# Kernel optimization log

Hardware: AMD Instinct MI355X
Metric: run time of the kernel (lower is better)

The kernel has to match this reference:

```python
import jax, jax.numpy as jnp
import numpy as np

N, E, D = 20000, 320000, 512


def _gat(x, W, a_src, a_dst, bias, src, dst, n, heads, ch):
    # PyG GATConv (eval mode, add_self_loops already applied via src/dst)
    h = (x @ W).reshape(n, heads, ch)              # [n, H, C]
    es = (h * a_src).sum(-1)                       # [n, H]
    ed = (h * a_dst).sum(-1)                       # [n, H]
    e = jax.nn.leaky_relu(es[src] + ed[dst], 0.2)  # [E, H]
    # edge-softmax grouped by destination node
    m = jax.ops.segment_max(e, dst, num_segments=n)
    ex = jnp.exp(e - m[dst])
    z = jax.ops.segment_sum(ex, dst, num_segments=n)
    alpha = ex / (z[dst] + 1e-16)                  # [E, H]
    out = jax.ops.segment_sum(h[src] * alpha[:, :, None], dst, num_segments=n)
    return out.reshape(n, heads * ch) + bias


def _ln(x, g, b):
    mu = x.mean(-1, keepdims=True)
    v = ((x - mu) ** 2).mean(-1, keepdims=True)
    return (x - mu) * jax.lax.rsqrt(v + 1e-5) * g + b


def setup_inputs() -> dict:
    key = jax.random.key(0)
    ks = jax.random.split(key, 24)
    p = lambda k, shape: jax.random.normal(k, shape, dtype=jnp.float32) * 0.05
    inp = {
        'x': jax.random.normal(ks[0], (N, D), dtype=jnp.float32),
        'edge_index': jax.random.randint(ks[1], (2, E), 0, N, dtype=jnp.int32),
        # GAT layer 1: 512 -> 8 heads x 128
        'w1': p(ks[2], (D, 1024)), 'as1': p(ks[3], (8, 128)), 'ad1': p(ks[4], (8, 128)), 'b1': jnp.zeros((1024,), jnp.float32),
        'g1': jnp.ones((1024,), jnp.float32), 'be1': jnp.zeros((1024,), jnp.float32),
        # GAT layer 2: 1024 -> 4 heads x 64
        'w2': p(ks[5], (1024, 256)), 'as2': p(ks[6], (4, 64)), 'ad2': p(ks[7], (4, 64)), 'b2': jnp.zeros((256,), jnp.float32),
        'g2': jnp.ones((256,), jnp.float32), 'be2': jnp.zeros((256,), jnp.float32),
        # GAT layer 3: 256 -> 2 heads x 32
        'w3': p(ks[8], (256, 64)), 'as3': p(ks[9], (2, 32)), 'ad3': p(ks[10], (2, 32)), 'b3': jnp.zeros((64,), jnp.float32),
        'g3': jnp.ones((64,), jnp.float32), 'be3': jnp.zeros((64,), jnp.float32),
        # anomaly scorer MLP
        'sw1': p(ks[11], (64, 64)), 'sb1': jnp.zeros((64,), jnp.float32),
        'sg1': jnp.ones((64,), jnp.float32), 'sbe1': jnp.zeros((64,), jnp.float32),
        'sw2': p(ks[12], (64, 32)), 'sb2': jnp.zeros((32,), jnp.float32),
        'sg2': jnp.ones((32,), jnp.float32), 'sbe2': jnp.zeros((32,), jnp.float32),
        'sw3': p(ks[13], (32, 1)), 'sb3': jnp.zeros((1,), jnp.float32),
    }
    return inp


def reference(x, edge_index, w1, as1, ad1, b1, g1, be1,
              w2, as2, ad2, b2, g2, be2,
              w3, as3, ad3, b3, g3, be3,
              sw1, sb1, sg1, sbe1, sw2, sb2, sg2, sbe2, sw3, sb3):
    loops = jnp.arange(N, dtype=edge_index.dtype)
    src = jnp.concatenate([edge_index[0], loops])  # add self-loops (PyG default)
    dst = jnp.concatenate([edge_index[1], loops])

    h1 = jax.nn.relu(_gat(x, w1, as1, ad1, b1, src, dst, N, 8, 128))
    h1 = _ln(h1, g1, be1)
    h2 = jax.nn.relu(_gat(h1, w2, as2, ad2, b2, src, dst, N, 4, 64))
    h2 = _ln(h2, g2, be2)
    h2 = h2 + h1[:, :256]
    h3 = jax.nn.relu(_gat(h2, w3, as3, ad3, b3, src, dst, N, 2, 32))
    h3 = _ln(h3, g3, be3)
    h3 = h3 + h2[:, :64]

    s = jax.nn.relu(h3 @ sw1 + sb1)
    s = _ln(s, sg1, sbe1)
    s = jax.nn.relu(s @ sw2 + sb2)
    s = _ln(s, sg2, sbe2)
    return jax.nn.sigmoid(s @ sw3 + sb3)  # [N, 1]
```

## Files before the change

kernel.cpp:

```cpp
#include <hip/hip_runtime.h>
#include <hip/hip_bf16.h>
#include <hip/hip_fp16.h>
#include <cstdint>

#define NN 20000
#define EE 320000
#define ETOT (EE + NN)

using f32x4 = __attribute__((ext_vector_type(4))) float;
using f16x8 = __attribute__((ext_vector_type(8))) _Float16;
typedef unsigned short ushortT;

__global__ __launch_bounds__(256) void preproc_kernel(
    const float* __restrict__ x, __half* __restrict__ x16,
    const float* __restrict__ w1, ushortT* __restrict__ w1t,
    const float* __restrict__ w2, ushortT* __restrict__ w2t,
    const float* __restrict__ w3, ushortT* __restrict__ w3t,
    const int* __restrict__ ei, int* __restrict__ deg)
{
  constexpr int N0 = NN * 512;
  constexpr int N1 = 512 * 1024;
  constexpr int N2 = 1024 * 256;
  constexpr int N3 = 256 * 64;
  constexpr int TOT = N0 + N1 + N2 + N3 + ETOT;
  for (int i = blockIdx.x * 256 + threadIdx.x; i < TOT; i += gridDim.x * 256) {
    int j = i;
    if (j < N0) { x16[j] = __float2half(x[j]); continue; }
    j -= N0;
    if (j < N1) {
      int k = j >> 10, c = j & 1023;
      w1t[(size_t)c * 512 + k] = __half_as_ushort(__float2half(w1[j]));
      continue;
    }
    j -= N1;
    if (j < N2) {
      int k = j >> 8, c = j & 255;
      w2t[(size_t)c * 1024 + k] = __half_as_ushort(__float2half(w2[j]));
      continue;
    }
    j -= N2;
    if (j < N3) {
      int k = j >> 6, c = j & 63;
      w3t[(size_t)c * 256 + k] = __half_as_ushort(__float2half(w3[j]));
      continue;
    }
    j -= N3;
    int d = (j < EE) ? ei[EE + j] : (j - EE);
    atomicAdd(&deg[d], 1);
  }
}

__global__ __launch_bounds__(1024) void scan_kernel(const int* __restrict__ deg,
                                                    int* __restrict__ row_ptr,
                                                    int* __restrict__ cursor) {
  __shared__ int partial[1024];
  const int t = threadIdx.x;
  constexpr int PER = (NN + 1023) / 1024;
  const int base = t * PER;
  int vals[PER];
  int local = 0;
  #pragma unroll
  for (int j = 0; j < PER; ++j) {
    int i = base + j;
    int v = (i < NN) ? deg[i] : 0;
    vals[j] = v; local += v;
  }
  partial[t] = local;
  __syncthreads();
  for (int off = 1; off < 1024; off <<= 1) {
    int x = (t >= off) ? partial[t - off] : 0;
    __syncthreads();
    partial[t] += x;
    __syncthreads();
  }
  int prefix = partial[t] - local;
  #pragma unroll
  for (int j = 0; j < PER; ++j) {
    int i = base + j;
    if (i < NN) { row_ptr[i] = prefix; cursor[i] = prefix; }
    prefix += vals[j];
  }
  if (t == 1023) row_ptr[NN] = prefix;
}

__global__ void scatter_kernel(const int* __restrict__ ei, int* __restrict__ cursor,
                               int* __restrict__ csr_src) {
  int i = blockIdx.x * 256 + threadIdx.x;
  if (i >= ETOT) return;
  int s, d;
  if (i < EE) { s = ei[i]; d = ei[EE + i]; } else { s = d = i - EE; }
  int pos = atomicAdd(&cursor[d], 1);
  csr_src[pos] = s;
}

__device__ __forceinline__ void gload16(const void* g, void* l) {
  __builtin_amdgcn_global_load_lds((const __attribute__((address_space(1))) void*)g,
                                   (__attribute__((address_space(3))) void*)l, 16, 0, 0);
}

template<int N> __device__ __forceinline__ void wait_vm() {
  if constexpr (N == 0) asm volatile("s_waitcnt vmcnt(0)" ::: "memory");
  else if constexpr (N == 2) asm volatile("s_waitcnt vmcnt(2)" ::: "memory");
  else if constexpr (N == 3) asm volatile("s_waitcnt vmcnt(3)" ::: "memory");
  else if constexpr (N == 4) asm volatile("s_waitcnt vmcnt(4)" ::: "memory");
  else if constexpr (N == 6) asm volatile("s_waitcnt vmcnt(6)" ::: "memory");
  else if constexpr (N == 8) asm volatile("s_waitcnt vmcnt(8)" ::: "memory");
  else static_assert(N <= 8, "unsupported vmcnt");
}

template<int BM, int BN, int FM, int FN, int CHEAD>
__global__ __launch_bounds__(256) void gemm_f16(
    const __half* __restrict__ A,
    const ushortT* __restrict__ Bt,
    __half* __restrict__ C, int M, int Ncols, int K,
    const float* __restrict__ asrc, const float* __restrict__ adst,
    float* __restrict__ es_g, float* __restrict__ ed_g, int H)
{
  constexpr int BK   = 32;
  constexpr int HALF = (BM + BN) * BK;
  constexpr int NL   = (BM * 4 + BN * 4) / 256;
  __shared__ ushortT lds[2 * HALF];

  const int tid  = threadIdx.x;
  const int lane = tid & 63;
  const int wid  = tid >> 6;
  const int wm   = (wid >> 1) * (FM * 16);
  const int wn   = (wid & 1) * (FN * 16);
  const int row0 = blockIdx.x * BM;
  const int col0 = blockIdx.y * BN;
  const int r    = lane & 15;
  const int kg   = lane >> 4;

  const ushortT* Au = (const ushortT*)A;

  auto STAGE = [&](int buf, int k0) {
    ushortT* sA = lds + buf * HALF;
    ushortT* sB = sA + BM * BK;
    #pragma unroll
    for (int i = tid; i < BM * 4; i += 256) {
      int row = i >> 2, slot = i & 3;
      int gs = slot ^ (row & 3);
      int grow = row0 + row; if (grow > M - 1) grow = M - 1;
      gload16(Au + (size_t)grow * K + k0 + gs * 8, sA + row * BK + slot * 8);
    }
    #pragma unroll
    for (int i = tid; i < BN * 4; i += 256) {
      int row = i >> 2, slot = i & 3;
      int gs = slot ^ (row & 3);
      gload16(Bt + (size_t)(col0 + row) * K + k0 + gs * 8, sB + row * BK + slot * 8);
    }
  };

  f32x4 acc[FM][FN] = {};
  const int nt = K / BK;

  STAGE(0, 0);
  for (int t = 0; t < nt; ++t) {
    if (t + 1 < nt) { STAGE((t + 1) & 1, (t + 1) * BK); wait_vm<NL>(); }
    else            { wait_vm<0>(); }
    __builtin_amdgcn_s_barrier();
    __builtin_amdgcn_sched_barrier(0);

    const ushortT* sA = lds + (t & 1) * HALF;
    const ushortT* sB = sA + BM * BK;
    const int ks = (kg ^ (r & 3)) * 8;
    f16x8 a[FM], b[FN];
    #pragma unroll
    for (int mi = 0; mi < FM; ++mi)
      a[mi] = *(const f16x8*)(sA + (wm + mi * 16 + r) * BK + ks);
    #pragma unroll
    for (int ni = 0; ni < FN; ++ni)
      b[ni] = *(const f16x8*)(sB + (wn + ni * 16 + r) * BK + ks);
    #pragma unroll
    for (int mi = 0; mi < FM; ++mi)
      #pragma unroll
      for (int ni = 0; ni < FN; ++ni)
        acc[mi][ni] = __builtin_amdgcn_mfma_f32_16x16x32_f16(a[mi], b[ni], acc[mi][ni], 0, 0, 0);
    __builtin_amdgcn_sched_barrier(0);
    __builtin_amdgcn_s_barrier();
  }

  #pragma unroll
  for (int mi = 0; mi < FM; ++mi) {
    int rb = row0 + wm + mi * 16 + (lane >> 4) * 4;
    #pragma unroll
    for (int ni = 0; ni < FN; ++ni) {
      int cc = col0 + wn + ni * 16 + (lane & 15);
      #pragma unroll
      for (int j = 0; j < 4; ++j) {
        int rr = rb + j;
        if (rr < M) C[(size_t)rr * Ncols + cc] = __float2half(acc[mi][ni][j]);
      }
    }
  }

  constexpr bool DIRECT = (CHEAD == FN * 16);
  float av[FN], dv[FN];
  #pragma unroll
  for (int ni = 0; ni < FN; ++ni) {
    int cc = col0 + wn + ni * 16 + (lane & 15);
    av[ni] = asrc[cc];
    dv[ni] = adst[cc];
  }
  float ps[FM][4], pd[FM][4];
  #pragma unroll
  for (int mi = 0; mi < FM; ++mi)
    #pragma unroll
    for (int j = 0; j < 4; ++j) {
      float s = 0.f, d = 0.f;
      #pragma unroll
      for (int ni = 0; ni < FN; ++ni) {
        float v = acc[mi][ni][j];
        s += v * av[ni];
        d += v * dv[ni];
      }
      #pragma unroll
      for (int off = 8; off; off >>= 1) {
        s += __shfl_xor(s, off);
        d += __shfl_xor(d, off);
      }
      ps[mi][j] = s; pd[mi][j] = d;
    }
  const int head = (col0 + wn) / CHEAD;
  if constexpr (DIRECT) {
    if ((lane & 15) == 0) {
      #pragma unroll
      for (int mi = 0; mi < FM; ++mi)
        #pragma unroll
        for (int j = 0; j < 4; ++j) {
          int rr = row0 + wm + mi * 16 + (lane >> 4) * 4 + j;
          if (rr < M) { es_g[rr * H + head] = ps[mi][j]; ed_g[rr * H + head] = pd[mi][j]; }
        }
    }
  } else {
    float* l_es = (float*)lds;
    float* l_ed = l_es + BM;
    __syncthreads();
    if ((wid & 1) == 0 && (lane & 15) == 0) {
      #pragma unroll
      for (int mi = 0; mi < FM; ++mi)
        #pragma unroll
        for (int j = 0; j < 4; ++j) {
          int rl = wm + mi * 16 + (lane >> 4) * 4 + j;
          l_es[rl] = ps[mi][j]; l_ed[rl] = pd[mi][j];
        }
    }
    __syncthreads();
    if ((wid & 1) == 1 && (lane & 15) == 0) {
      #pragma unroll
      for (int mi = 0; mi < FM; ++mi)
        #pragma unroll
        for (int j = 0; j < 4; ++j) {
          int rl = wm + mi * 16 + (lane >> 4) * 4 + j;
          int rr = row0 + rl;
          if (rr < M) {
            es_g[rr * H + head] = ps[mi][j] + l_es[rl];
            ed_g[rr * H + head] = pd[mi][j] + l_ed[rl];
          }
        }
    }
  }
}

template<int VPT> struct GVec;
template<> struct GVec<16> { uint4 a, b; };
template<> struct GVec<4>  { uint2 a; };
template<> struct GVec<1>  { ushortT a; };

template<int VPT>
__device__ __forceinline__ GVec<VPT> gload(const __half* p) {
  GVec<VPT> v;
  if constexpr (VPT == 16) { v.a = *(const uint4*)p; v.b = *(const uint4*)(p + 8); }
  else if constexpr (VPT == 4) { v.a = *(const uint2*)p; }
  else { v.a = *(const ushortT*)p; }
  return v;
}

template<int VPT>
__device__ __forceinline__ void gfma(const GVec<VPT>& u, float w, float* acc) {
  if constexpr (VPT == 1) {
    __half hv;
    *(ushortT*)&hv = u.a;
    acc[0] += w * __half2float(hv);
  } else {
    const __half2* p = (const __half2*)&u;
    #pragma unroll
    for (int j = 0; j < VPT / 2; ++j) {
      float2 f = __half22float2(p[j]);
      acc[2 * j]     += w * f.x;
      acc[2 * j + 1] += w * f.y;
    }
  }
}

template<int H, int C, bool RES_IN, bool F16_OUT, bool SCORER, int WPB>
__global__ __launch_bounds__(WPB * 64) void gat_agg_wave(
    const __half* __restrict__ h, const float* __restrict__ es_g, const float* __restrict__ ed_g,
    const int* __restrict__ row_ptr, const int* __restrict__ csr_src,
    const float* __restrict__ bias, const float* __restrict__ gamma, const float* __restrict__ beta,
    const __half* __restrict__ res_in, int res_stride, __half* __restrict__ out_h,
    const float* __restrict__ sw1, const float* __restrict__ sb1,
    const float* __restrict__ sg1, const float* __restrict__ sbe1,
    const float* __restrict__ sw2, const float* __restrict__ sb2,
    const float* __restrict__ sg2, const float* __restrict__ sbe2,
    const float* __restrict__ sw3, const float* __restrict__ sb3,
    float* __restrict__ out)
{
  constexpr int HC   = H * C;
  constexpr int VPT  = HC / 64;
  constexpr int CH   = 32;
  constexpr int BB   = 4;
  constexpr int LOGH = (H == 8) ? 3 : ((H == 4) ? 2 : 1);
  constexpr int EPR  = 64 >> LOGH;
  constexpr int ROUNDS = CH / EPR;
  constexpr int WST  = CH + 4;

  const int wave = threadIdx.x >> 6;
  const int lane = threadIdx.x & 63;
  const int n    = blockIdx.x * WPB + wave;
  const int c0   = lane * VPT;
  const int myh  = c0 / C;
  const int wh   = lane & (H - 1);

  __shared__ int   s_lds[WPB][CH];
  __shared__ float w_lds[WPB][H * WST];
  int*   sl = s_lds[wave];
  float* wl = w_lds[wave];

  const int p0 = row_ptr[n];
  const int p1 = row_ptr[n + 1];
  const float edw = ed_g[n * H + wh];

  float acc[VPT];
  #pragma unroll
  for (int j = 0; j < VPT; ++j) acc[j] = 0.f;
  float z = 0.f;

  for (int base = p0; base < p1; base += CH) {
    const int m = min(CH, p1 - base);
    if (lane < CH) sl[lane] = (base + lane < p1) ? csr_src[base + lane] : n;
    #pragma unroll
    for (int rr = 0; rr < ROUNDS; ++rr) {
      int e = (lane >> LOGH) + rr * EPR;
      int s = sl[e];
      float w = 0.f;
      if (base + e < p1) {
        float ev = es_g[s * H + wh] + edw;
        ev = (ev >= 0.f) ? ev : 0.2f * ev;
        w = __expf(ev);
      }
      wl[wh * WST + e] = w;
    }

    const int nb = m / BB;
    GVec<VPT> uA[BB], uB[BB];
    float4 wA, wB;

    auto LOADB = [&](int b, GVec<VPT> (&u)[BB], float4& w4) {
      int4 s4 = *(const int4*)&sl[b * BB];
      w4 = *(const float4*)&wl[myh * WST + b * BB];
      u[0] = gload<VPT>(h + (size_t)s4.x * HC + c0);
      u[1] = gload<VPT>(h + (size_t)s4.y * HC + c0);
      u[2] = gload<VPT>(h + (size_t)s4.z * HC + c0);
      u[3] = gload<VPT>(h + (size_t)s4.w * HC + c0);
    };
    auto FMAB = [&](GVec<VPT> (&u)[BB], float4& w4) {
      z += w4.x + w4.y + w4.z + w4.w;
      gfma<VPT>(u[0], w4.x, acc);
      gfma<VPT>(u[1], w4.y, acc);
      gfma<VPT>(u[2], w4.z, acc);
      gfma<VPT>(u[3], w4.w, acc);
    };

    if (nb > 0) LOADB(0, uA, wA);
    #pragma unroll
    for (int bb = 0; bb < CH / BB; bb += 2) {
      if (bb < nb) {
        if (bb + 1 < nb) LOADB(bb + 1, uB, wB);
        FMAB(uA, wA);
      }
      if (bb + 1 < nb) {
        if (bb + 2 < nb) LOADB(bb + 2, uA, wA);
        FMAB(uB, wB);
      }
    }
    for (int e = nb * BB; e < m; ++e) {
      int s = sl[e];
      float w = wl[myh * WST + e];
      z += w;
      GVec<VPT> u = gload<VPT>(h + (size_t)s * HC + c0);
      gfma<VPT>(u, w, acc);
    }
  }

  float inv = 1.f / (z + 1e-16f);
  float ov[VPT];
  float psum = 0.f, psq = 0.f;
  #pragma unroll
  for (int j = 0; j < VPT; ++j) {
    float x = fmaxf(acc[j] * inv + bias[c0 + j], 0.f);
    ov[j] = x; psum += x; psq += x * x;
  }
  #pragma unroll
  for (int o = 32; o > 0; o >>= 1) {
    psum += __shfl_xor(psum, o);
    psq  += __shfl_xor(psq, o);
  }
  float mu  = psum / (float)HC;
  float var = psq / (float)HC - mu * mu;
  float rs  = rsqrtf(var + 1e-5f);

  ushortT hb[VPT > 1 ? VPT : 2];
  #pragma unroll
  for (int j = 0; j < VPT; ++j) {
    int c = c0 + j;
    float o = (ov[j] - mu) * rs * gamma[c] + beta[c];
    if constexpr (RES_IN) o += __half2float(res_in[(size_t)n * res_stride + c]);
    ov[j] = o;
    if constexpr (F16_OUT) hb[j] = __half_as_ushort(__float2half(o));
  }
  if constexpr (F16_OUT) {
    ushortT* po = (ushortT*)out_h + (size_t)n * HC + c0;
    if constexpr (VPT == 16) {
      *(uint4*)po       = *(uint4*)&hb[0];
      *(uint4*)(po + 8) = *(uint4*)&hb[8];
    } else if constexpr (VPT == 4) {
      *(uint2*)po = *(uint2*)&hb[0];
    } else {
      *po = hb[0];
    }
  }

  if constexpr (SCORER) {
    wl[lane] = ov[0];
    float s1 = sb1[lane];
    #pragma unroll 16
    for (int k = 0; k < 64; ++k) s1 += wl[k] * sw1[k * 64 + lane];
    s1 = fmaxf(s1, 0.f);
    float su = s1, sq = s1 * s1;
    #pragma unroll
    for (int o = 32; o > 0; o >>= 1) { su += __shfl_xor(su, o); sq += __shfl_xor(sq, o); }
    float mu1 = su * (1.f / 64.f), var1 = sq * (1.f / 64.f) - mu1 * mu1;
    float v1 = (s1 - mu1) * rsqrtf(var1 + 1e-5f) * sg1[lane] + sbe1[lane];
    wl[lane] = v1;
    float o2 = 0.f;
    if (lane < 32) {
      o2 = sb2[lane];
      #pragma unroll 16
      for (int k = 0; k < 64; ++k) o2 += wl[k] * sw2[k * 32 + lane];
      o2 = fmaxf(o2, 0.f);
    }
    float su2 = o2, sq2 = o2 * o2;
    #pragma unroll
    for (int o = 16; o > 0; o >>= 1) { su2 += __shfl_xor(su2, o); sq2 += __shfl_xor(sq2, o); }
    float p = 0.f;
    if (lane < 32) {
      float mu2 = su2 * (1.f / 32.f), var2 = sq2 * (1.f / 32.f) - mu2 * mu2;
      float v2 = (o2 - mu2) * rsqrtf(var2 + 1e-5f) * sg2[lane] + sbe2[lane];
      p = v2 * sw3[lane];
    }
    #pragma unroll
    for (int o = 16; o > 0; o >>= 1) p += __shfl_xor(p, o);
    if (lane == 0) out[n] = 1.f / (1.f + expf(-(p + sb3[0])));
  }
}

extern "C" void kernel_launch(void* const* d_in, const int* in_sizes, int n_in,
                              void* d_out, int out_size, void* d_ws, size_t ws_size,
                              hipStream_t stream)
{
  const float* x    = (const float*)d_in[0];
  const int*   ei   = (const int*)d_in[1];
  const float* w1   = (const float*)d_in[2];
  const float* as1  = (const float*)d_in[3];
  const float* ad1  = (const float*)d_in[4];
  const float* b1   = (const float*)d_in[5];
  const float* g1v  = (const float*)d_in[6];
  const float* be1  = (const float*)d_in[7];
  const float* w2   = (const float*)d_in[8];
  const float* as2  = (const float*)d_in[9];
  const float* ad2  = (const float*)d_in[10];
  const float* b2   = (const float*)d_in[11];
  const float* g2v  = (const float*)d_in[12];
  const float* be2  = (const float*)d_in[13];
  const float* w3   = (const float*)d_in[14];
  const float* as3  = (const float*)d_in[15];
  const float* ad3  = (const float*)d_in[16];
  const float* b3   = (const float*)d_in[17];
  const float* g3v  = (const float*)d_in[18];
  const float* be3  = (const float*)d_in[19];
  const float* sw1  = (const float*)d_in[20];
  const float* sb1  = (const float*)d_in[21];
  const float* sg1  = (const float*)d_in[22];
  const float* sbe1 = (const float*)d_in[23];
  const float* sw2  = (const float*)d_in[24];
  const float* sb2  = (const float*)d_in[25];
  const float* sg2  = (const float*)d_in[26];
  const float* sbe2 = (const float*)d_in[27];
  const float* sw3  = (const float*)d_in[28];
  const float* sb3  = (const float*)d_in[29];
  float* out = (float*)d_out;

  char* ws = (char*)d_ws;
  size_t off = 0;
  auto alloc = [&](size_t bytes) -> void* {
    off = (off + 255) & ~(size_t)255;
    void* p = ws + off;
    off += bytes;
    return p;
  };

  __half*  h_gemm  = (__half*)alloc((size_t)NN * 1024 * 2);
  __half*  h1_f16  = (__half*)alloc((size_t)NN * 1024 * 2);
  __half*  h2_f16  = (__half*)alloc((size_t)NN * 256 * 2);
  __half*  x16     = (__half*)alloc((size_t)NN * 512 * 2);
  ushortT* w1t     = (ushortT*)alloc((size_t)512 * 1024 * 2);
  ushortT* w2t     = (ushortT*)alloc((size_t)1024 * 256 * 2);
  ushortT* w3t     = (ushortT*)alloc((size_t)256 * 64 * 2);
  float*   es_buf  = (float*)alloc((size_t)NN * 8 * 4);
  float*   ed_buf  = (float*)alloc((size_t)NN * 8 * 4);
  int*     deg     = (int*)alloc((size_t)NN * 4);
  int*     row_ptr = (int*)alloc((size_t)(NN + 1) * 4);
  int*     cursor  = (int*)alloc((size_t)NN * 4);
  int*     csr_src = (int*)alloc((size_t)ETOT * 4);
  (void)ws_size; (void)in_sizes; (void)n_in; (void)out_size;

  hipMemsetAsync(deg, 0, (size_t)NN * 4, stream);
  preproc_kernel<<<2048, 256, 0, stream>>>(x, x16, w1, w1t, w2, w2t, w3, w3t, ei, deg);
  scan_kernel<<<1, 1024, 0, stream>>>(deg, row_ptr, cursor);
  scatter_kernel<<<(ETOT + 255) / 256, 256, 0, stream>>>(ei, cursor, csr_src);

  const int MB = (NN + 127) / 128;

  gemm_f16<128, 128, 4, 4, 128><<<dim3(MB, 1024 / 128), 256, 0, stream>>>(
      x16, w1t, h_gemm, NN, 1024, 512, as1, ad1, es_buf, ed_buf, 8);
  gat_agg_wave<8, 128, false, true, false, 8><<<NN / 8, 512, 0, stream>>>(
      h_gemm, es_buf, ed_buf, row_ptr, csr_src, b1, g1v, be1,
      nullptr, 0, h1_f16,
      nullptr, nullptr, nullptr, nullptr, nullptr, nullptr, nullptr, nullptr, nullptr, nullptr, nullptr);

  gemm_f16<128, 128, 4, 4, 64><<<dim3(MB, 256 / 128), 256, 0, stream>>>(
      h1_f16, w2t, h_gemm, NN, 256, 1024, as2, ad2, es_buf, ed_buf, 4);
  gat_agg_wave<4, 64, true, true, false, 8><<<NN / 8, 512, 0, stream>>>(
      h_gemm, es_buf, ed_buf, row_ptr, csr_src, b2, g2v, be2,
      h1_f16, 1024, h2_f16,
      nullptr, nullptr, nullptr, nullptr, nullptr, nullptr, nullptr, nullptr, nullptr, nullptr, nullptr);

  gemm_f16<128, 64, 4, 2, 32><<<dim3(MB, 1), 256, 0, stream>>>(
      h2_f16, w3t, h_gemm, NN, 64, 256, as3, ad3, es_buf, ed_buf, 2);
  gat_agg_wave<2, 32, true, false, true, 8><<<NN / 8, 512, 0, stream>>>(
      h_gemm, es_buf, ed_buf, row_ptr, csr_src, b3, g3v, be3,
      h2_f16, 256, nullptr,
      sw1, sb1, sg1, sbe1, sw2, sb2, sg2, sbe2, sw3, sb3, out);
}
```

Before: 325.8 us.

## Split wave into edge groups for narrow GAT layers to widen gathers

Adds a group parameter G so that, in the narrower layers 2 and 3, one wave is split into G lane groups. Each group handles a different subset of a node's edges using wider vector loads, and the partial sums are combined with xor shuffles at the end. This gives more gathers in flight per wave and removes scalar 2-byte loads for layer 3. Blocks also shrink from 8 waves to 4, with a launch-bounds occupancy hint. The cost is extra cross-lane reductions, and the LayerNorm statistics now count every group, relying on the combined values being identical in each group.

After: 327.6 us. About the same (+0.6%).

```diff
diff --git a/kernel.cpp b/kernel.cpp
--- a/kernel.cpp
+++ b/kernel.cpp
@@ -264,37 +264,31 @@
 
 template<int VPT> struct GVec;
 template<> struct GVec<16> { uint4 a, b; };
+template<> struct GVec<8>  { uint4 a; };
 template<> struct GVec<4>  { uint2 a; };
-template<> struct GVec<1>  { ushortT a; };
 
 template<int VPT>
 __device__ __forceinline__ GVec<VPT> gload(const __half* p) {
   GVec<VPT> v;
   if constexpr (VPT == 16) { v.a = *(const uint4*)p; v.b = *(const uint4*)(p + 8); }
-  else if constexpr (VPT == 4) { v.a = *(const uint2*)p; }
-  else { v.a = *(const ushortT*)p; }
+  else if constexpr (VPT == 8) { v.a = *(const uint4*)p; }
+  else { v.a = *(const uint2*)p; }
   return v;
 }
 
 template<int VPT>
 __device__ __forceinline__ void gfma(const GVec<VPT>& u, float w, float* acc) {
-  if constexpr (VPT == 1) {
-    __half hv;
-    *(ushortT*)&hv = u.a;
-    acc[0] += w * __half2float(hv);
-  } else {
-    const __half2* p = (const __half2*)&u;
-    #pragma unroll
-    for (int j = 0; j < VPT / 2; ++j) {
-      float2 f = __half22float2(p[j]);
-      acc[2 * j]     += w * f.x;
-      acc[2 * j + 1] += w * f.y;
-    }
-  }
-}
-
-template<int H, int C, bool RES_IN, bool F16_OUT, bool SCORER, int WPB>
-__global__ __launch_bounds__(WPB * 64) void gat_agg_wave(
+  const __half2* p = (const __half2*)&u;
+  #pragma unroll
+  for (int j = 0; j < VPT / 2; ++j) {
+    float2 f = __half22float2(p[j]);
+    acc[2 * j]     += w * f.x;
+    acc[2 * j + 1] += w * f.y;
+  }
+}
+
+template<int H, int C, int G, bool RES_IN, bool F16_OUT, bool SCORER, int WPB>
+__global__ __launch_bounds__(WPB * 64, 2) void gat_agg_wave(
     const __half* __restrict__ h, const float* __restrict__ es_g, const float* __restrict__ ed_g,
     const int* __restrict__ row_ptr, const int* __restrict__ csr_src,
     const float* __restrict__ bias, const float* __restrict__ gamma, const float* __restrict__ beta,
@@ -307,7 +301,8 @@
     float* __restrict__ out)
 {
   constexpr int HC   = H * C;
-  constexpr int VPT  = HC / 64;
+  constexpr int LPG  = 64 / G;
+  constexpr int VPT  = HC / LPG;
   constexpr int CH   = 32;
   constexpr int BB   = 4;
   constexpr int LOGH = (H == 8) ? 3 : ((H == 4) ? 2 : 1);
@@ -315,15 +310,17 @@
   constexpr int ROUNDS = CH / EPR;
   constexpr int WST  = CH + 4;
 
-  const int wave = threadIdx.x >> 6;
-  const int lane = threadIdx.x & 63;
-  const int n    = blockIdx.x * WPB + wave;
-  const int c0   = lane * VPT;
-  const int myh  = c0 / C;
-  const int wh   = lane & (H - 1);
+  const int wave  = threadIdx.x >> 6;
+  const int lane  = threadIdx.x & 63;
+  const int grp   = lane / LPG;
+  const int glane = lane % LPG;
+  const int n     = blockIdx.x * WPB + wave;
+  const int c0    = glane * VPT;
+  const int myh   = c0 / C;
+  const int wh    = lane & (H - 1);
 
   __shared__ int   s_lds[WPB][CH];
-  __shared__ float w_lds[WPB][H * WST];
+  __shared__ float w_lds[WPB][(H * WST < 64) ? 64 : H * WST];
   int*   sl = s_lds[wave];
   float* wl = w_lds[wave];
 
@@ -352,44 +349,83 @@
       wl[wh * WST + e] = w;
     }
 
-    const int nb = m / BB;
-    GVec<VPT> uA[BB], uB[BB];
-    float4 wA, wB;
-
-    auto LOADB = [&](int b, GVec<VPT> (&u)[BB], float4& w4) {
-      int4 s4 = *(const int4*)&sl[b * BB];
-      w4 = *(const float4*)&wl[myh * WST + b * BB];
-      u[0] = gload<VPT>(h + (size_t)s4.x * HC + c0);
-      u[1] = gload<VPT>(h + (size_t)s4.y * HC + c0);
-      u[2] = gload<VPT>(h + (size_t)s4.z * HC + c0);
-      u[3] = gload<VPT>(h + (size_t)s4.w * HC + c0);
-    };
-    auto FMAB = [&](GVec<VPT> (&u)[BB], float4& w4) {
-      z += w4.x + w4.y + w4.z + w4.w;
-      gfma<VPT>(u[0], w4.x, acc);
-      gfma<VPT>(u[1], w4.y, acc);
-      gfma<VPT>(u[2], w4.z, acc);
-      gfma<VPT>(u[3], w4.w, acc);
-    };
-
-    if (nb > 0) LOADB(0, uA, wA);
-    #pragma unroll
-    for (int bb = 0; bb < CH / BB; bb += 2) {
-      if (bb < nb) {
-        if (bb + 1 < nb) LOADB(bb + 1, uB, wB);
-        FMAB(uA, wA);
-      }
-      if (bb + 1 < nb) {
-        if (bb + 2 < nb) LOADB(bb + 2, uA, wA);
-        FMAB(uB, wB);
-      }
-    }
-    for (int e = nb * BB; e < m; ++e) {
-      int s = sl[e];
-      float w = wl[myh * WST + e];
-      z += w;
-      GVec<VPT> u = gload<VPT>(h + (size_t)s * HC + c0);
-      gfma<VPT>(u, w, acc);
+    if constexpr (G == 1) {
+      const int nb = m / BB;
+      GVec<VPT> uA[BB], uB[BB];
+      float4 wA, wB;
+      auto LOADB = [&](int b, GVec<VPT> (&u)[BB], float4& w4) {
+        int4 s4 = *(const int4*)&sl[b * BB];
+        w4 = *(const float4*)&wl[myh * WST + b * BB];
+        u[0] = gload<VPT>(h + (size_t)s4.x * HC + c0);
+        u[1] = gload<VPT>(h + (size_t)s4.y * HC + c0);
+        u[2] = gload<VPT>(h + (size_t)s4.z * HC + c0);
+        u[3] = gload<VPT>(h + (size_t)s4.w * HC + c0);
+      };
+      auto FMAB = [&](GVec<VPT> (&u)[BB], float4& w4) {
+        z += w4.x + w4.y + w4.z + w4.w;
+        gfma<VPT>(u[0], w4.x, acc);
+        gfma<VPT>(u[1], w4.y, acc);
+        gfma<VPT>(u[2], w4.z, acc);
+        gfma<VPT>(u[3], w4.w, acc);
+      };
+      if (nb > 0) LOADB(0, uA, wA);
+      #pragma unroll
+      for (int bb = 0; bb < CH / BB; bb += 2) {
+        if (bb < nb) {
+          if (bb + 1 < nb) LOADB(bb + 1, uB, wB);
+          FMAB(uA, wA);
+        }
+        if (bb + 1 < nb) {
+          if (bb + 2 < nb) LOADB(bb + 2, uA, wA);
+          FMAB(uB, wB);
+        }
+      }
+      for (int e = nb * BB; e < m; ++e) {
+        int s = sl[e];
+        float w = wl[myh * WST + e];
+        z += w;
+        GVec<VPT> u = gload<VPT>(h + (size_t)s * HC + c0);
+        gfma<VPT>(u, w, acc);
+      }
+    } else {
+      const int kG = (m + G - 1) / G;
+      GVec<VPT> uA[2], uB[2];
+      float wA[2], wB[2];
+      auto LOADP = [&](int k, GVec<VPT> (&u)[2], float (&w)[2]) {
+        #pragma unroll
+        for (int t = 0; t < 2; ++t) {
+          int kk = k + t;
+          bool ok = kk < kG;
+          int e = ok ? (kk * G + grp) : 0;
+          int s = sl[e];
+          w[t] = ok ? wl[myh * WST + e] : 0.f;
+          u[t] = gload<VPT>(h + (size_t)s * HC + c0);
+        }
+      };
+      auto FMAP = [&](GVec<VPT> (&u)[2], float (&w)[2]) {
+        z += w[0] + w[1];
+        gfma<VPT>(u[0], w[0], acc);
+        gfma<VPT>(u[1], w[1], acc);
+      };
+      const int np = (kG + 1) >> 1;
+      if (np > 0) LOADP(0, uA, wA);
+      for (int p = 0; p < np; p += 2) {
+        if (p + 1 < np) LOADP((p + 1) * 2, uB, wB);
+        FMAP(uA, wA);
+        if (p + 1 < np) {
+          if (p + 2 < np) LOADP((p + 2) * 2, uA, wA);
+          FMAP(uB, wB);
+        }
+      }
+    }
+  }
+
+  if constexpr (G > 1) {
+    #pragma unroll
+    for (int o = LPG; o < 64; o <<= 1) {
+      #pragma unroll
+      for (int j = 0; j < VPT; ++j) acc[j] += __shfl_xor(acc[j], o);
+      z += __shfl_xor(z, o);
     }
   }
 
@@ -406,33 +442,40 @@
     psum += __shfl_xor(psum, o);
     psq  += __shfl_xor(psq, o);
   }
-  float mu  = psum / (float)HC;
-  float var = psq / (float)HC - mu * mu;
+  float mu  = psum / (float)(HC * G);
+  float var = psq / (float)(HC * G) - mu * mu;
   float rs  = rsqrtf(var + 1e-5f);
 
-  ushortT hb[VPT > 1 ? VPT : 2];
+  ushortT hb[VPT];
   #pragma unroll
   for (int j = 0; j < VPT; ++j) {
     int c = c0 + j;
     float o = (ov[j] - mu) * rs * gamma[c] + beta[c];
-    if constexpr (RES_IN) o += __half2float(res_in[(size_t)n * res_stride + c]);
+    if constexpr (RES_IN) {
+      if (grp == 0) o += __half2float(res_in[(size_t)n * res_stride + c]);
+    }
     ov[j] = o;
     if constexpr (F16_OUT) hb[j] = __half_as_ushort(__float2half(o));
   }
   if constexpr (F16_OUT) {
-    ushortT* po = (ushortT*)out_h + (size_t)n * HC + c0;
-    if constexpr (VPT == 16) {
-      *(uint4*)po       = *(uint4*)&hb[0];
-      *(uint4*)(po + 8) = *(uint4*)&hb[8];
-    } else if constexpr (VPT == 4) {
-      *(uint2*)po = *(uint2*)&hb[0];
-    } else {
-      *po = hb[0];
+    if (grp == 0) {
+      ushortT* po = (ushortT*)out_h + (size_t)n * HC + c0;
+      if constexpr (VPT == 16) {
+        *(uint4*)po       = *(uint4*)&hb[0];
+        *(uint4*)(po + 8) = *(uint4*)&hb[8];
+      } else if constexpr (VPT == 8) {
+        *(uint4*)po = *(uint4*)&hb[0];
+      } else {
+        *(uint2*)po = *(uint2*)&hb[0];
+      }
     }
   }
 
   if constexpr (SCORER) {
-    wl[lane] = ov[0];
+    if (grp == 0) {
+      #pragma unroll
+      for (int j = 0; j < VPT; ++j) wl[c0 + j] = ov[j];
+    }
     float s1 = sb1[lane];
     #pragma unroll 16
     for (int k = 0; k < 64; ++k) s1 += wl[k] * sw1[k * 64 + lane];
@@ -534,21 +577,21 @@
 
   gemm_f16<128, 128, 4, 4, 128><<<dim3(MB, 1024 / 128), 256, 0, stream>>>(
       x16, w1t, h_gemm, NN, 1024, 512, as1, ad1, es_buf, ed_buf, 8);
-  gat_agg_wave<8, 128, false, true, false, 8><<<NN / 8, 512, 0, stream>>>(
+  gat_agg_wave<8, 128, 1, false, true, false, 4><<<NN / 4, 256, 0, stream>>>(
       h_gemm, es_buf, ed_buf, row_ptr, csr_src, b1, g1v, be1,
       nullptr, 0, h1_f16,
       nullptr, nullptr, nullptr, nullptr, nullptr, nullptr, nullptr, nullptr, nullptr, nullptr, nullptr);
 
   gemm_f16<128, 128, 4, 4, 64><<<dim3(MB, 256 / 128), 256, 0, stream>>>(
       h1_f16, w2t, h_gemm, NN, 256, 1024, as2, ad2, es_buf, ed_buf, 4);
-  gat_agg_wave<4, 64, true, true, false, 8><<<NN / 8, 512, 0, stream>>>(
+  gat_agg_wave<4, 64, 2, true, true, false, 4><<<NN / 4, 256, 0, stream>>>(
       h_gemm, es_buf, ed_buf, row_ptr, csr_src, b2, g2v, be2,
       h1_f16, 1024, h2_f16,
       nullptr, nullptr, nullptr, nullptr, nullptr, nullptr, nullptr, nullptr, nullptr, nullptr, nullptr);
 
   gemm_f16<128, 64, 4, 2, 32><<<dim3(MB, 1), 256, 0, stream>>>(
       h2_f16, w3t, h_gemm, NN, 64, 256, as3, ad3, es_buf, ed_buf, 2);
-  gat_agg_wave<2, 32, true, false, true, 8><<<NN / 8, 512, 0, stream>>>(
+  gat_agg_wave<2, 32, 8, true, false, true, 4><<<NN / 4, 256, 0, stream>>>(
       h_gemm, es_buf, ed_buf, row_ptr, csr_src, b3, g3v, be3,
       h2_f16, 256, nullptr,
       sw1, sb1, sg1, sbe1, sw2, sb2, sg2, sbe2, sw3, sb3, out);
```
